# Optimization experiments

Hardware: AMD Instinct MI355X
Metric: run time of the kernel (lower is better)

Reference implementation:

```python
import jax, jax.numpy as jnp
import numpy as np

B, T, HH, WW, D, NH, MLPD, KH, KW = 2, 16, 24, 24, 128, 4, 512, 5, 5
T_ = T + 1
HW = HH * WW
SIZE = KH * KW
PH, PW = KH // 2, KW // 2


def _ln(x, w, b):
    m = x.mean(-1, keepdims=True)
    v = ((x - m) ** 2).mean(-1, keepdims=True)
    return (x - m) / jnp.sqrt(v + 1e-5) * w + b


def _mha(q, kv, mask, Wq, bq, Wk, bk, Wv, bv, Wo, bo):
    # q: (N, Lq, D), kv: (N, Lk, D), mask: (N, Lq|1, Lk) True = masked
    N, Lq, Dm = q.shape
    dh = Dm // NH
    qh = (q @ Wq + bq).reshape(N, Lq, NH, dh).transpose(0, 2, 1, 3)
    kh = (kv @ Wk + bk).reshape(N, -1, NH, dh).transpose(0, 2, 1, 3)
    vh = (kv @ Wv + bv).reshape(N, -1, NH, dh).transpose(0, 2, 1, 3)
    scores = jnp.einsum('nhqd,nhkd->nhqk', qh, kh) * (1.0 / np.sqrt(dh))
    logits = jnp.where(mask[:, None, :, :], -1e9, scores)
    attn = jax.nn.softmax(logits, axis=-1)
    out = jnp.einsum('nhqk,nhkd->nhqd', attn, vh).transpose(0, 2, 1, 3).reshape(N, Lq, Dm)
    return out @ Wo + bo, logits


def _unfold_patches(x):
    # x: (N, H, W, D) -> (N, H, W, SIZE, D), kernel positions row-major (matches F.unfold)
    xp = jnp.pad(x, ((0, 0), (PH, PH), (PW, PW), (0, 0)))
    return jnp.stack([xp[:, i:i + HH, j:j + WW, :] for i in range(KH) for j in range(KW)], axis=3)


def setup_inputs() -> dict:
    key = jax.random.key(0)
    ks = iter(jax.random.split(key, 48))
    w = lambda *s: jax.random.normal(next(ks), s, jnp.float32) * 0.02
    inp = {
        'query': jax.random.normal(next(ks), (B, T_, HW, D), jnp.float32),
        'spatial_mask': jnp.zeros((1,), bool),  # ignored by the module
        'temporal_mask': jnp.zeros((B * HW, T_, T_), bool),
        'ln_s_w': jnp.ones((D,), jnp.float32), 'ln_s_b': jnp.zeros((D,), jnp.float32),
        'sWq': w(D, D), 'sbq': jnp.zeros((D,), jnp.float32),
        'sWk': w(D, D), 'sbk': jnp.zeros((D,), jnp.float32),
        'sWv': w(D, D), 'sbv': jnp.zeros((D,), jnp.float32),
        'sWo': w(D, D), 'sbo': jnp.zeros((D,), jnp.float32),
        'ln_t_w': jnp.ones((D,), jnp.float32), 'ln_t_b': jnp.zeros((D,), jnp.float32),
        'tWq': w(D, D), 'tbq': jnp.zeros((D,), jnp.float32),
        'tWk': w(D, D), 'tbk': jnp.zeros((D,), jnp.float32),
        'tWv': w(D, D), 'tbv': jnp.zeros((D,), jnp.float32),
        'tWo': w(D, D), 'tbo': jnp.zeros((D,), jnp.float32),
        'ln_m_w': jnp.ones((D,), jnp.float32), 'ln_m_b': jnp.zeros((D,), jnp.float32),
        'mW1': w(D, MLPD), 'mb1': jnp.zeros((MLPD,), jnp.float32),
        'mW2': w(MLPD, D), 'mb2': jnp.zeros((D,), jnp.float32),
    }
    return inp


def reference(query, spatial_mask, temporal_mask, ln_s_w, ln_s_b, sWq, sbq, sWk, sbk, sWv, sbv, sWo, sbo,
              ln_t_w, ln_t_b, tWq, tbq, tWk, tbk, tWv, tbv, tWo, tbo, ln_m_w, ln_m_b, mW1, mb1, mW2, mb2):
    # ---- spatial branch (local window attention + global CLS key) ----
    visual = query[:, 1:].reshape(B * T, HH, WW, D)
    neigh = _unfold_patches(visual).reshape(B * T * HW, SIZE, D)
    vis = visual.reshape(B * T * HW, 1, D)
    cls = query[:, 0].mean(axis=1, keepdims=True)              # (B,1,D)
    cls_rep = jnp.tile(cls, (T * HW, 1, 1))                    # faithful to torch .repeat ordering
    kv = jnp.concatenate([cls_rep, neigh], axis=1)             # (N, SIZE+1, D)
    # padding mask: True where neighbor falls outside the frame (faithful: CLS zero-col appended LAST)
    valid = jnp.pad(jnp.ones((HH, WW), bool), ((PH, PH), (PW, PW)))
    mpat = jnp.stack([valid[i:i + HH, j:j + WW] for i in range(KH) for j in range(KW)], axis=2).reshape(HW, SIZE)
    smask = jnp.concatenate([~mpat, jnp.zeros((HW, 1), bool)], axis=1)           # (HW, SIZE+1)
    smask = jnp.broadcast_to(smask[None], (B * T, HW, SIZE + 1)).reshape(B * T * HW, 1, SIZE + 1)
    out, _ = _mha(_ln(vis, ln_s_w, ln_s_b), _ln(kv, ln_s_w, ln_s_b), smask,
                  sWq, sbq, sWk, sbk, sWv, sbv, sWo, sbo)
    x = out + vis
    x = jnp.concatenate([query[:, 0:1], x.reshape(B, T, HW, D)], axis=1)  # (B, T_, HW, D)
    # ---- temporal branch ----
    xt = x.transpose(0, 2, 1, 3).reshape(B * HW, T_, D)
    xn = _ln(xt, ln_t_w, ln_t_b)
    x_, logits = _mha(xn, xn, temporal_mask, tWq, tbq, tWk, tbk, tWv, tbv, tWo, tbo)
    xt = x_ + xt
    x = xt.reshape(B, HW, T_, D).transpose(0, 2, 1, 3)
    x = x.at[:, 0].set(x[:, 0:1].mean(axis=2))                 # average CLS across spatial locations
    logits = logits.reshape(B, HW, NH, T_, T_)
    # ---- MLP ----
    h = _ln(x, ln_m_w, ln_m_b)
    h = jax.nn.gelu(h @ mW1 + mb1, approximate=False) @ mW2 + mb2
    x = h + x
    return x, logits
```

## Files before the change

kernel.cpp:

```cpp
#include <hip/hip_runtime.h>
#include <math.h>

#define BB    2
#define TT    16
#define TP    17
#define HH_   24
#define WW_   24
#define HWW   576
#define DD    128
#define NHH   4
#define MLPD_ 512
#define NPIX  18432
#define NTOK  19584
#define SCALE 0.17677669529663688f
#define OUT0_SIZE 2506752

typedef unsigned short u16;
typedef __bf16 bf16x8 __attribute__((ext_vector_type(8)));
typedef float f32x4 __attribute__((ext_vector_type(4)));

__device__ __forceinline__ u16 f2b(float f) {
  unsigned u = __float_as_uint(f);
  u += 0x7FFFu + ((u >> 16) & 1u);
  return (u16)(u >> 16);
}
__device__ __forceinline__ float blo(unsigned u) { return __uint_as_float(u << 16); }
__device__ __forceinline__ float bhi(unsigned u) { return __uint_as_float(u & 0xFFFF0000u); }
__device__ __forceinline__ float b2f(u16 u) { return __uint_as_float((unsigned)u << 16); }

__device__ __forceinline__ float dot8p(uint4 a, uint4 b) {
  float s = blo(a.x) * blo(b.x) + bhi(a.x) * bhi(b.x);
  s += blo(a.y) * blo(b.y) + bhi(a.y) * bhi(b.y);
  s += blo(a.z) * blo(b.z) + bhi(a.z) * bhi(b.z);
  s += blo(a.w) * blo(b.w) + bhi(a.w) * bhi(b.w);
  return s;
}
__device__ __forceinline__ float getp(const float4* P, int j) {
  float4 v = P[j >> 2];
  switch (j & 3) { case 0: return v.x; case 1: return v.y; case 2: return v.z; default: return v.w; }
}
__device__ __forceinline__ void gld_lds16(const void* g, void* l) {
  __builtin_amdgcn_global_load_lds(
      (const __attribute__((address_space(1))) void*)g,
      (__attribute__((address_space(3))) void*)l, 16, 0, 0);
}

#define QLN8_BODY(SP, Q8, LNW, LNB, EMIT)                                        \
  {                                                                              \
    const float4* s4_ = (const float4*)(SP) + (Q8) * 4;                          \
    float4 xv_[4];                                                               \
    float sum_ = 0.f, sq_ = 0.f;                                                 \
    _Pragma("unroll")                                                            \
    for (int i_ = 0; i_ < 4; i_++) {                                             \
      float4 a_ = s4_[i_]; xv_[i_] = a_;                                         \
      sum_ += (a_.x + a_.y) + (a_.z + a_.w);                                     \
      sq_  += a_.x * a_.x + a_.y * a_.y + a_.z * a_.z + a_.w * a_.w;             \
    }                                                                            \
    sum_ += __shfl_xor(sum_, 1, 8); sum_ += __shfl_xor(sum_, 2, 8);              \
    sum_ += __shfl_xor(sum_, 4, 8);                                              \
    sq_  += __shfl_xor(sq_, 1, 8);  sq_  += __shfl_xor(sq_, 2, 8);               \
    sq_  += __shfl_xor(sq_, 4, 8);                                               \
    float mean_ = sum_ * (1.0f / DD);                                            \
    float inv_ = rsqrtf(sq_ * (1.0f / DD) - mean_ * mean_ + 1e-5f);              \
    const float4* w4_ = (const float4*)(LNW) + (Q8) * 4;                         \
    const float4* b4_ = (const float4*)(LNB) + (Q8) * 4;                         \
    _Pragma("unroll")                                                            \
    for (int i_ = 0; i_ < 2; i_++) {                                             \
      float4 a0_ = xv_[2 * i_], a1_ = xv_[2 * i_ + 1];                           \
      float4 w0_ = w4_[2 * i_], w1_ = w4_[2 * i_ + 1];                           \
      float4 c0_ = b4_[2 * i_], c1_ = b4_[2 * i_ + 1];                           \
      uint4 o_;                                                                  \
      o_.x = (unsigned)f2b((a0_.x - mean_) * inv_ * w0_.x + c0_.x)               \
           | ((unsigned)f2b((a0_.y - mean_) * inv_ * w0_.y + c0_.y) << 16);      \
      o_.y = (unsigned)f2b((a0_.z - mean_) * inv_ * w0_.z + c0_.z)               \
           | ((unsigned)f2b((a0_.w - mean_) * inv_ * w0_.w + c0_.w) << 16);      \
      o_.z = (unsigned)f2b((a1_.x - mean_) * inv_ * w1_.x + c1_.x)               \
           | ((unsigned)f2b((a1_.y - mean_) * inv_ * w1_.y + c1_.y) << 16);      \
      o_.w = (unsigned)f2b((a1_.z - mean_) * inv_ * w1_.z + c1_.z)               \
           | ((unsigned)f2b((a1_.w - mean_) * inv_ * w1_.w + c1_.w) << 16);      \
      EMIT(i_, o_);                                                              \
    }                                                                            \
  }

#define QLN_BODY(SP, Q, LNW, LNB, EMIT)                                          \
  {                                                                              \
    const float4* s4_ = (const float4*)(SP) + (Q) * 8;                           \
    float4 xv_[8];                                                               \
    float sum_ = 0.f, sq_ = 0.f;                                                 \
    _Pragma("unroll")                                                            \
    for (int i_ = 0; i_ < 8; i_++) {                                             \
      float4 a_ = s4_[i_]; xv_[i_] = a_;                                         \
      sum_ += (a_.x + a_.y) + (a_.z + a_.w);                                     \
      sq_  += a_.x * a_.x + a_.y * a_.y + a_.z * a_.z + a_.w * a_.w;             \
    }                                                                            \
    sum_ += __shfl_xor(sum_, 1, 4); sum_ += __shfl_xor(sum_, 2, 4);              \
    sq_  += __shfl_xor(sq_, 1, 4);  sq_  += __shfl_xor(sq_, 2, 4);               \
    float mean_ = sum_ * (1.0f / DD);                                            \
    float inv_ = rsqrtf(sq_ * (1.0f / DD) - mean_ * mean_ + 1e-5f);              \
    const float4* w4_ = (const float4*)(LNW) + (Q) * 8;                          \
    const float4* b4_ = (const float4*)(LNB) + (Q) * 8;                          \
    _Pragma("unroll")                                                            \
    for (int i_ = 0; i_ < 4; i_++) {                                             \
      float4 a0_ = xv_[2 * i_], a1_ = xv_[2 * i_ + 1];                           \
      float4 w0_ = w4_[2 * i_], w1_ = w4_[2 * i_ + 1];                           \
      float4 c0_ = b4_[2 * i_], c1_ = b4_[2 * i_ + 1];                           \
      uint4 o_;                                                                  \
      o_.x = (unsigned)f2b((a0_.x - mean_) * inv_ * w0_.x + c0_.x)               \
           | ((unsigned)f2b((a0_.y - mean_) * inv_ * w0_.y + c0_.y) << 16);      \
      o_.y = (unsigned)f2b((a0_.z - mean_) * inv_ * w0_.z + c0_.z)               \
           | ((unsigned)f2b((a0_.w - mean_) * inv_ * w0_.w + c0_.w) << 16);      \
      o_.z = (unsigned)f2b((a1_.x - mean_) * inv_ * w1_.x + c1_.x)               \
           | ((unsigned)f2b((a1_.y - mean_) * inv_ * w1_.y + c1_.y) << 16);      \
      o_.w = (unsigned)f2b((a1_.z - mean_) * inv_ * w1_.z + c1_.z)               \
           | ((unsigned)f2b((a1_.w - mean_) * inv_ * w1_.w + c1_.w) << 16);      \
      EMIT(i_, o_);                                                              \
    }                                                                            \
  }

#define MFMA_64x128(ASP, BSP, WR, WC, LANE, ACC)                                 \
  _Pragma("unroll")                                                              \
  for (int kc_ = 0; kc_ < 4; kc_++) {                                            \
    int kob_ = (kc_ * 32 + ((LANE) >> 4) * 8) * 2;                               \
    bf16x8 af_[2], bf_[2];                                                       \
    _Pragma("unroll")                                                            \
    for (int i_ = 0; i_ < 2; i_++) {                                             \
      int ra_ = (WR) * 32 + i_ * 16 + ((LANE) & 15);                             \
      af_[i_] = *(const bf16x8*)((const char*)(ASP) + ((ra_ * 256 + kob_) ^ ((ra_ & 7) << 4))); \
      int rb_ = (WC) * 32 + i_ * 16 + ((LANE) & 15);                             \
      bf_[i_] = *(const bf16x8*)((const char*)(BSP) + ((rb_ * 256 + kob_) ^ ((rb_ & 7) << 4))); \
    }                                                                            \
    _Pragma("unroll")                                                            \
    for (int i_ = 0; i_ < 2; i_++)                                               \
      _Pragma("unroll")                                                          \
      for (int j_ = 0; j_ < 2; j_++)                                             \
        ACC[i_][j_] = __builtin_amdgcn_mfma_f32_16x16x32_bf16(af_[i_], bf_[j_], ACC[i_][j_], 0, 0, 0); \
  }

__global__ void k_packprep(const float* w0, const float* w1, const float* w2, const float* w3,
                           const float* w4, const float* w5, const float* w6, const float* w7,
                           const float* w8, const float* w9,
                           const float* sbq, const float* sbk, const float* sbv,
                           const float* tbq, const float* tbk, const float* tbv,
                           const float* query, const float* ln_w, const float* ln_b,
                           u16* __restrict__ out, float* __restrict__ sb3, float* __restrict__ tb3,
                           u16* __restrict__ KCb, u16* __restrict__ VCb) {
  int bid = blockIdx.x, tid = threadIdx.x;
  if (bid < 1027) {
    int idx = bid * 256 + tid;
    if (idx < 131072) {
      int seg = idx >> 14, local = idx & 16383;
      const float* tbl[8] = {w0, w1, w2, w3, w4, w5, w6, w7};
      int kk = local >> 7, nn = local & 127;
      out[seg * 16384 + nn * 128 + kk] = f2b(tbl[seg][local]);
    } else if (idx < 196608) {
      int local = idx - 131072;
      int kk = local >> 9, nn = local & 511;
      out[131072 + nn * 128 + kk] = f2b(w8[local]);
    } else if (idx < 262144) {
      int local = idx - 196608;
      int kk = local >> 7, nn = local & 127;
      out[196608 + nn * 512 + kk] = f2b(w9[local]);
    } else if (idx < 262528) {
      int i = idx - 262144;
      sb3[i] = i < 128 ? sbq[i] : (i < 256 ? sbk[i - 128] : sbv[i - 256]);
    } else if (idx < 262912) {
      int i = idx - 262528;
      tb3[i] = i < 128 ? tbq[i] : (i < 256 ? tbk[i - 128] : tbv[i - 256]);
    }
    return;
  }
  __shared__ float part[2][DD];
  __shared__ float xr[DD];
  __shared__ float pk[2][DD], pv[2][DD];
  int r = bid - 1027;
  int c = tid >> 7, d = tid & 127;
  if (r < BB) {
    const float* base = query + (size_t)r * TP * HWW * DD + d;
    float s = 0.f;
    for (int hw = c * 288; hw < c * 288 + 288; ++hw) s += base[(size_t)hw * DD];
    part[c][d] = s;
    __syncthreads();
    if (tid < DD) part[0][tid] = (part[0][tid] + part[1][tid]) * (1.0f / HWW);
    __syncthreads();
    if (tid < DD) {
      float mean = 0.f;
      for (int i = 0; i < DD; i++) mean += part[0][i];
      mean *= (1.0f / DD);
      float var = 0.f;
      for (int i = 0; i < DD; i++) { float t = part[0][i] - mean; var += t * t; }
      var *= (1.0f / DD);
      xr[tid] = (part[0][tid] - mean) * rsqrtf(var + 1e-5f) * ln_w[tid] + ln_b[tid];
    }
  } else {
    if (tid < DD) xr[tid] = ln_b[tid];
  }
  __syncthreads();
  float sk = 0.f, sv = 0.f;
  for (int e = c * 64; e < c * 64 + 64; e++) {
    float xe = xr[e];
    sk += xe * w1[e * DD + d];
    sv += xe * w2[e * DD + d];
  }
  pk[c][d] = sk; pv[c][d] = sv;
  __syncthreads();
  if (tid < DD) {
    float k = pk[0][tid] + pk[1][tid] + sbk[tid];
    float v = pv[0][tid] + pv[1][tid] + sbv[tid];
    KCb[r * DD + tid] = f2b(k);
    VCb[r * DD + tid] = f2b(v);
  }
}

__global__ __launch_bounds__(256, 2) void k_gemm(
    const float* __restrict__ Av, const float* __restrict__ lnw, const float* __restrict__ lnb,
    const u16* __restrict__ Wt, const float* __restrict__ bias,
    u16* __restrict__ Cb, int ldc) {
  __shared__ __align__(16) u16 As[64 * 128];
  __shared__ __align__(16) u16 Bs[128 * 128];
  int tx = threadIdx.x;
  int row0 = blockIdx.x * 64, col0 = blockIdx.y * 128;
  int lane = tx & 63, wid = tx >> 6;
  f32x4 z = {0.f, 0.f, 0.f, 0.f};
  f32x4 acc[2][4];
#pragma unroll
  for (int i = 0; i < 2; i++)
#pragma unroll
    for (int j = 0; j < 4; j++) acc[i][j] = z;

  {
    int rloc = tx >> 2, q = tx & 3;
    int r = row0 + rloc;
    int b2 = r / (TT * HWW); int r2 = r - b2 * (TT * HWW);
    const float* sp = Av + ((size_t)b2 * TP * HWW + HWW + r2) * DD;
#define EMIT_AS(i_, o_) { int dstb = (rloc * 256 + q * 64 + (i_) * 16) ^ ((rloc & 7) << 4); \
                          *(uint4*)((char*)As + dstb) = o_; }
    QLN_BODY(sp, q, lnw, lnb, EMIT_AS)
#undef EMIT_AS
  }
#pragma unroll
  for (int t = 0; t < 8; t++) {
    int ci = t * 256 + tx;
    int r = ci >> 4;
    int c16 = (ci ^ (r & 7)) & 15;
    gld_lds16(&Wt[(size_t)(col0 + r) * 128 + c16 * 8], (char*)Bs + ci * 16);
  }
  __syncthreads();
#pragma unroll
  for (int kc = 0; kc < 4; kc++) {
    int kob = (kc * 32 + (lane >> 4) * 8) * 2;
    bf16x8 af[2], bfr[4];
#pragma unroll
    for (int i = 0; i < 2; i++) {
      int ra = (wid >> 1) * 32 + i * 16 + (lane & 15);
      af[i] = *(const bf16x8*)((const char*)As + ((ra * 256 + kob) ^ ((ra & 7) << 4)));
    }
#pragma unroll
    for (int j = 0; j < 4; j++) {
      int rb = (wid & 1) * 64 + j * 16 + (lane & 15);
      bfr[j] = *(const bf16x8*)((const char*)Bs + ((rb * 256 + kob) ^ ((rb & 7) << 4)));
    }
#pragma unroll
    for (int i = 0; i < 2; i++)
#pragma unroll
      for (int j = 0; j < 4; j++)
        acc[i][j] = __builtin_amdgcn_mfma_f32_16x16x32_bf16(af[i], bfr[j], acc[i][j], 0, 0, 0);
  }

  int rbase = row0 + (wid >> 1) * 32 + (lane >> 4) * 4;
  int cbase = col0 + (wid & 1) * 64 + (lane & 15);
#pragma unroll
  for (int i = 0; i < 2; i++)
#pragma unroll
    for (int e = 0; e < 4; e++) {
      int r = rbase + i * 16 + e;
#pragma unroll
      for (int j = 0; j < 4; j++) {
        int c = cbase + j * 16;
        Cb[(size_t)r * ldc + c] = f2b(acc[i][j][e] + bias[c]);
      }
    }
}

__global__ __launch_bounds__(512, 2) void k_f1(
    const u16* __restrict__ S0b, const float* __restrict__ query,
    const u16* __restrict__ WT, const float* __restrict__ sbo, const float* __restrict__ tb3,
    const float* __restrict__ lnw, const float* __restrict__ lnb,
    float* __restrict__ XB, u16* __restrict__ QKVb) {
  __shared__ __align__(16) char smem[50176];
  u16* As  = (u16*)smem;
  u16* Bs  = (u16*)(smem + 16384);
  float* L = (float*)smem;
  u16* As2 = (u16*)(smem + 33792);
  u16* Bs2 = (u16*)smem;
  int tx = threadIdx.x, bid = blockIdx.x;
  int lane = tx & 63, wid = tx >> 6;
  int wr = (wid >> 2) & 1, wc = wid & 3;
  f32x4 z = {0.f, 0.f, 0.f, 0.f};
  int rb0 = wr * 32 + (lane >> 4) * 4;
  int cb0 = wc * 32 + (lane & 15);
  size_t row0T;

  if (bid < 288) {
    int row0P = bid * 64;
    int b2 = row0P / (TT * HWW);
    row0T = (size_t)row0P + (size_t)(b2 + 1) * HWW;
#pragma unroll
    for (int t = 0; t < 2; t++) {
      int ci = t * 512 + tx; int r = ci >> 4; int c16 = (ci ^ (r & 7)) & 15;
      gld_lds16(&S0b[(size_t)(row0P + r) * 128 + c16 * 8], (char*)As + ci * 16);
    }
    const u16* Wo = WT + 49152;
#pragma unroll
    for (int t = 0; t < 4; t++) {
      int ci = t * 512 + tx; int r = ci >> 4; int c16 = (ci ^ (r & 7)) & 15;
      gld_lds16(&Wo[(size_t)r * 128 + c16 * 8], (char*)Bs + ci * 16);
    }
    __syncthreads();
    f32x4 acc[2][2];
#pragma unroll
    for (int i = 0; i < 2; i++)
#pragma unroll
      for (int j = 0; j < 2; j++) acc[i][j] = z;
    MFMA_64x128(As, Bs, wr, wc, lane, acc)
    __syncthreads();
#pragma unroll
    for (int i = 0; i < 2; i++)
#pragma unroll
      for (int e = 0; e < 4; e++) {
        int r = rb0 + i * 16 + e;
#pragma unroll
        for (int j = 0; j < 2; j++) {
          int c = cb0 + j * 16;
          float v = acc[i][j][e] + sbo[c] + query[(row0T + r) * DD + c];
          XB[(row0T + r) * DD + c] = v;
          L[r * 132 + c] = v;
        }
      }
    __syncthreads();
    int rloc = tx >> 3, q8 = tx & 7;
    const float* sp = L + rloc * 132;
#define EMIT_AS2(i_, o_) { int dstb = (rloc * 256 + q8 * 32 + (i_) * 16) ^ ((rloc & 7) << 4); \
                           *(uint4*)((char*)As2 + dstb) = o_; }
    QLN8_BODY(sp, q8, lnw, lnb, EMIT_AS2)
#undef EMIT_AS2
  } else {
    int pb = bid - 288;
    row0T = (size_t)(pb / 9) * TP * HWW + (size_t)(pb % 9) * 64;
    int rloc = tx >> 3, q8 = tx & 7;
    const float* sp = query + (row0T + rloc) * DD;
#define EMIT_AS2(i_, o_) { int dstb = (rloc * 256 + q8 * 32 + (i_) * 16) ^ ((rloc & 7) << 4); \
                           *(uint4*)((char*)As2 + dstb) = o_; }
    QLN8_BODY(sp, q8, lnw, lnb, EMIT_AS2)
#undef EMIT_AS2
  }
  __syncthreads();

  const u16* Wq = WT + 65536;
  for (int by = 0; by < 3; by++) {
    if (by) __syncthreads();
#pragma unroll
    for (int t = 0; t < 4; t++) {
      int ci = t * 512 + tx; int r = ci >> 4; int c16 = (ci ^ (r & 7)) & 15;
      gld_lds16(&Wq[(size_t)(by * 128 + r) * 128 + c16 * 8], (char*)Bs2 + ci * 16);
    }
    __syncthreads();
    f32x4 acc[2][2];
#pragma unroll
    for (int i = 0; i < 2; i++)
#pragma unroll
      for (int j = 0; j < 2; j++) acc[i][j] = z;
    MFMA_64x128(As2, Bs2, wr, wc, lane, acc)
#pragma unroll
    for (int i = 0; i < 2; i++)
#pragma unroll
      for (int e = 0; e < 4; e++) {
        int r = rb0 + i * 16 + e;
#pragma unroll
        for (int j = 0; j < 2; j++) {
          int c = cb0 + j * 16;
          QKVb[(row0T + r) * 384 + by * 128 + c] = f2b(acc[i][j][e] + tb3[by * 128 + c]);
        }
      }
  }
}

__global__ __launch_bounds__(512, 2) void k_f2(
    const u16* __restrict__ S0b, const float* __restrict__ XB, const float* __restrict__ query,
    const u16* __restrict__ WT, const float* __restrict__ tbo,
    const float* __restrict__ mb1, const float* __restrict__ mb2,
    const float* __restrict__ lnw, const float* __restrict__ lnb,
    float* __restrict__ X2, float* __restrict__ out0) {
  __shared__ __align__(16) char smem[66560];
  u16* As  = (u16*)smem;
  u16* Bs  = (u16*)(smem + 16384);
  float* L = (float*)smem;
  u16* As2 = (u16*)(smem + 33792);
  u16* Ws  = (u16*)smem;
  u16* Hs  = (u16*)(smem + 50176);
  int tx = threadIdx.x, bid = blockIdx.x;
  int lane = tx & 63, wid = tx >> 6;
  int wr = (wid >> 2) & 1, wc = wid & 3;
  bool isV = bid < 288;
  size_t row0T = isV ? ((size_t)(bid / 144) * TP * HWW + HWW + (size_t)(bid % 144) * 64)
                     : ((size_t)((bid - 288) / 9) * TP * HWW + (size_t)((bid - 288) % 9) * 64);
  f32x4 z = {0.f, 0.f, 0.f, 0.f};
  int rb0 = wr * 32 + (lane >> 4) * 4;
  int cb0 = wc * 32 + (lane & 15);

#pragma unroll
  for (int t = 0; t < 2; t++) {
    int ci = t * 512 + tx; int r = ci >> 4; int c16 = (ci ^ (r & 7)) & 15;
    gld_lds16(&S0b[(row0T + r) * 128 + c16 * 8], (char*)As + ci * 16);
  }
  const u16* Wo = WT + 114688;
#pragma unroll
  for (int t = 0; t < 4; t++) {
    int ci = t * 512 + tx; int r = ci >> 4; int c16 = (ci ^ (r & 7)) & 15;
    gld_lds16(&Wo[(size_t)r * 128 + c16 * 8], (char*)Bs + ci * 16);
  }
  __syncthreads();
  f32x4 acc[2][2];
#pragma unroll
  for (int i = 0; i < 2; i++)
#pragma unroll
    for (int j = 0; j < 2; j++) acc[i][j] = z;
  MFMA_64x128(As, Bs, wr, wc, lane, acc)
  __syncthreads();

  f32x4 xres[2][2];
  const float* res = isV ? XB : query;
#pragma unroll
  for (int i = 0; i < 2; i++)
#pragma unroll
    for (int e = 0; e < 4; e++) {
      int r = rb0 + i * 16 + e;
#pragma unroll
      for (int j = 0; j < 2; j++) {
        int c = cb0 + j * 16;
        float v = acc[i][j][e] + tbo[c] + res[(row0T + r) * DD + c];
        xres[i][j][e] = v;
        if (isV) L[r * 132 + c] = v;
        else     X2[(row0T + r) * DD + c] = v;
      }
    }
  if (!isV) return;
  __syncthreads();
  {
    int rloc = tx >> 3, q8 = tx & 7;
    const float* sp = L + rloc * 132;
#define EMIT_AS2(i_, o_) { int dstb = (rloc * 256 + q8 * 32 + (i_) * 16) ^ ((rloc & 7) << 4); \
                           *(uint4*)((char*)As2 + dstb) = o_; }
    QLN8_BODY(sp, q8, lnw, lnb, EMIT_AS2)
#undef EMIT_AS2
  }
  __syncthreads();

  const u16* W1 = WT + 131072;
  const u16* W2 = WT + 196608;
  f32x4 accC[2][2];
#pragma unroll
  for (int i = 0; i < 2; i++)
#pragma unroll
    for (int j = 0; j < 2; j++) accC[i][j] = z;

  for (int nb = 0; nb < 4; nb++) {
    if (nb) __syncthreads();
#pragma unroll
    for (int t = 0; t < 4; t++) {
      int ci = t * 512 + tx; int r = ci >> 4; int c16 = (ci ^ (r & 7)) & 15;
      gld_lds16(&W1[(size_t)(nb * 128 + r) * 128 + c16 * 8], (char*)Ws + ci * 16);
    }
    __syncthreads();
    f32x4 accH[2][2];
#pragma unroll
    for (int i = 0; i < 2; i++)
#pragma unroll
      for (int j = 0; j < 2; j++) accH[i][j] = z;
    MFMA_64x128(As2, Ws, wr, wc, lane, accH)
    __syncthreads();
#pragma unroll
    for (int i = 0; i < 2; i++)
#pragma unroll
      for (int e = 0; e < 4; e++) {
        int hr = rb0 + i * 16 + e;
#pragma unroll
        for (int j = 0; j < 2; j++) {
          int hc = cb0 + j * 16;
          float v = accH[i][j][e] + mb1[nb * 128 + hc];
          v = 0.5f * v * (1.0f + erff(v * 0.70710678118654752f));
          *(u16*)((char*)Hs + ((hr * 256 + hc * 2) ^ ((hr & 7) << 4))) = f2b(v);
        }
      }
#pragma unroll
    for (int t = 0; t < 4; t++) {
      int ci = t * 512 + tx; int r = ci >> 4; int c16 = (ci ^ (r & 7)) & 15;
      gld_lds16(&W2[(size_t)r * 512 + nb * 128 + c16 * 8], (char*)Ws + ci * 16);
    }
    __syncthreads();
    MFMA_64x128(Hs, Ws, wr, wc, lane, accC)
  }

#pragma unroll
  for (int i = 0; i < 2; i++)
#pragma unroll
    for (int e = 0; e < 4; e++) {
      int r = rb0 + i * 16 + e;
#pragma unroll
      for (int j = 0; j < 2; j++) {
        int c = cb0 + j * 16;
        out0[(row0T + r) * DD + c] = accC[i][j][e] + mb2[c] + xres[i][j][e];
      }
    }
}

__global__ __launch_bounds__(256) void k_sattn(const u16* __restrict__ qkvb,
                                               const u16* __restrict__ KCb,
                                               const u16* __restrict__ VCb,
                                               u16* __restrict__ outb) {
  __shared__ float Ps[8][32];
  int tid = threadIdx.x;
  int g = tid >> 5, lj = tid & 31;
  int bid = blockIdx.x;
  int blk = (bid & 7) * 1152 + (bid >> 3);
  int G = blk * 8 + g;
  int n = G >> 2, h = G & 3;
  int f = n / HWW, hw = n - f * HWW;
  int hp = hw / WW_, wp = hw - hp * WW_;
  size_t FB = (size_t)f * HWW * 384;

  const u16* kp;
  bool masked;
  if (lj == 0) {
    kp = KCb + (n & 1) * DD + h * 32;
    masked = !(hp >= 2 && wp >= 2);
  } else {
    int k = lj - 1;
    int y = hp + k / 5 - 2, x = wp + k % 5 - 2;
    bool vok = ((unsigned)y < 24u) & ((unsigned)x < 24u) & (k < 25);
    kp = vok ? (qkvb + FB + (size_t)(y * WW_ + x) * 384 + 128 + h * 32)
             : (KCb + BB * DD + h * 32);
    if (lj < 25) { int ym = hp + lj / 5 - 2, xm = wp + lj % 5 - 2;
                   masked = !(((unsigned)ym < 24u) & ((unsigned)xm < 24u)); }
    else masked = false;
  }
  const uint4* q4p = (const uint4*)(qkvb + (size_t)n * 384 + h * 32);
  const uint4* k4p = (const uint4*)kp;
  float s = 0.f;
#pragma unroll
  for (int i = 0; i < 4; i++) s += dot8p(q4p[i], k4p[i]);

  float scr = masked ? -1e9f : s * SCALE;
  if (lj >= 26) scr = -1e30f;
  float mx = scr;
#pragma unroll
  for (int o = 16; o > 0; o >>= 1) mx = fmaxf(mx, __shfl_xor(mx, o, 32));
  float p = __expf(scr - mx);
  float sum = p;
#pragma unroll
  for (int o = 16; o > 0; o >>= 1) sum += __shfl_xor(sum, o, 32);
  Ps[g][lj] = p * (1.0f / sum);

  float4 P4[7];
#pragma unroll
  for (int i = 0; i < 7; i++) P4[i] = *(const float4*)&Ps[g][i * 4];

  float o = getp(P4, 0) * b2f(VCb[(n & 1) * DD + h * 32 + lj]);
#pragma unroll
  for (int k = 0; k < 25; k++) {
    int y = hp + k / 5 - 2, x = wp + k % 5 - 2;
    bool vok = ((unsigned)y < 24u) & ((unsigned)x < 24u);
    const u16* vp = vok ? (qkvb + FB + (size_t)(y * WW_ + x) * 384 + 256)
                        : (VCb + BB * DD);
    o += getp(P4, k + 1) * b2f(vp[h * 32 + lj]);
  }
  outb[(size_t)n * DD + h * 32 + lj] = f2b(o);
}

__global__ __launch_bounds__(256) void k_tattn(const u16* __restrict__ qkv,
                                               u16* __restrict__ outb,
                                               float* __restrict__ logits) {
  __shared__ float Qs[8][TP][32];
  __shared__ float Ps[8][TP][17];
  int tid = threadIdx.x;
  int g = tid >> 5, lj = tid & 31;
  int s = blockIdx.x * 2 + (g >> 2);
  int h = g & 3;
  int b = s / HWW, hw = s - b * HWW;
  size_t base = ((size_t)b * TP * HWW + hw) * 384 + h * 32;
  const size_t TSTR = (size_t)HWW * 384;

  float kreg[32];
  {
    const uint4* k4 = (const uint4*)(qkv + base + (size_t)(lj < 17 ? lj : 16) * TSTR + 128);
#pragma unroll
    for (int i = 0; i < 4; i++) {
      uint4 u = k4[i];
      kreg[i * 8 + 0] = blo(u.x); kreg[i * 8 + 1] = bhi(u.x);
      kreg[i * 8 + 2] = blo(u.y); kreg[i * 8 + 3] = bhi(u.y);
      kreg[i * 8 + 4] = blo(u.z); kreg[i * 8 + 5] = bhi(u.z);
      kreg[i * 8 + 6] = blo(u.w); kreg[i * 8 + 7] = bhi(u.w);
    }
  }
  float vreg[TP];
#pragma unroll
  for (int t = 0; t < TP; t++) {
    Qs[g][t][lj] = b2f(qkv[base + (size_t)t * TSTR + lj]);
    vreg[t]      = b2f(qkv[base + (size_t)t * TSTR + 256 + lj]);
  }

  float* lp = logits + (size_t)s * (NHH * TP * TP) + (size_t)h * (TP * TP);
#pragma unroll 4
  for (int tq = 0; tq < TP; tq++) {
    const float4* qrow = (const float4*)&Qs[g][tq][0];
    float a0 = 0.f, a1 = 0.f, a2 = 0.f, a3 = 0.f;
#pragma unroll
    for (int d4 = 0; d4 < 8; d4++) {
      float4 q4 = qrow[d4];
      a0 += q4.x * kreg[d4 * 4 + 0];
      a1 += q4.y * kreg[d4 * 4 + 1];
      a2 += q4.z * kreg[d4 * 4 + 2];
      a3 += q4.w * kreg[d4 * 4 + 3];
    }
    float sc = ((a0 + a1) + (a2 + a3)) * SCALE;
    if (lj < 17) lp[tq * 17 + lj] = sc;
    float scm = (lj < 17) ? sc : -1e30f;
    float mx = scm;
#pragma unroll
    for (int o = 16; o > 0; o >>= 1) mx = fmaxf(mx, __shfl_xor(mx, o, 32));
    float p = __expf(scm - mx);
    float sum = p;
#pragma unroll
    for (int o = 16; o > 0; o >>= 1) sum += __shfl_xor(sum, o, 32);
    if (lj < 17) Ps[g][tq][lj] = p * (1.0f / sum);
  }
#pragma unroll 4
  for (int tq = 0; tq < TP; tq++) {
    const float* prow = &Ps[g][tq][0];
    float o = 0.f;
#pragma unroll
    for (int t = 0; t < TP; t++) o += prow[t] * vreg[t];
    size_t r = ((size_t)b * TP + tq) * HWW + hw;
    outb[r * DD + h * 32 + lj] = f2b(o);
  }
}

__global__ void k_f3(const float* __restrict__ x2,
                     const float* __restrict__ mW1, const float* __restrict__ mb1,
                     const float* __restrict__ mW2, const float* __restrict__ mb2,
                     const float* __restrict__ lnw, const float* __restrict__ lnb,
                     float* __restrict__ out0) {
  __shared__ float part[4][DD];
  __shared__ float cls[DD];
  __shared__ float lnr[DD];
  __shared__ float H[MLPD_];
  __shared__ float orow[DD];
  int b = blockIdx.x, tid = threadIdx.x;
  int c = tid >> 7, d = tid & 127;
  const float* base = x2 + (size_t)b * TP * HWW * DD;
  float s = 0.f;
  for (int hw = c * 144; hw < c * 144 + 144; ++hw) s += base[(size_t)hw * DD + d];
  part[c][d] = s;
  __syncthreads();
  if (tid < DD) cls[tid] = (part[0][tid] + part[1][tid] + part[2][tid] + part[3][tid]) * (1.0f / HWW);
  __syncthreads();
  if (tid < DD) {
    float mean = 0.f;
    for (int i = 0; i < DD; i++) mean += cls[i];
    mean *= (1.0f / DD);
    float var = 0.f;
    for (int i = 0; i < DD; i++) { float t = cls[i] - mean; var += t * t; }
    var *= (1.0f / DD);
    lnr[tid] = (cls[tid] - mean) * rsqrtf(var + 1e-5f) * lnw[tid] + lnb[tid];
  }
  __syncthreads();
  {
    float a = mb1[tid];
    for (int k = 0; k < DD; k++) a += lnr[k] * mW1[k * MLPD_ + tid];
    H[tid] = 0.5f * a * (1.0f + erff(a * 0.70710678118654752f));
  }
  __syncthreads();
  if (tid < DD) {
    float a = mb2[tid];
    for (int k = 0; k < MLPD_; k++) a += H[k] * mW2[k * DD + tid];
    orow[tid] = a + cls[tid];
  }
  __syncthreads();
  float* ob = out0 + (size_t)b * TP * HWW * DD;
  for (int idx = tid; idx < HWW * DD; idx += 512) ob[idx] = orow[idx & 127];
}

extern "C" void kernel_launch(void* const* d_in, const int* in_sizes, int n_in,
                              void* d_out, int out_size, void* d_ws, size_t ws_size,
                              hipStream_t stream) {
  const float* query  = (const float*)d_in[0];
  const float* ln_s_w = (const float*)d_in[3];
  const float* ln_s_b = (const float*)d_in[4];
  const float* sWq = (const float*)d_in[5];  const float* sbq = (const float*)d_in[6];
  const float* sWk = (const float*)d_in[7];  const float* sbk = (const float*)d_in[8];
  const float* sWv = (const float*)d_in[9];  const float* sbv = (const float*)d_in[10];
  const float* sWo = (const float*)d_in[11]; const float* sbo = (const float*)d_in[12];
  const float* ln_t_w = (const float*)d_in[13];
  const float* ln_t_b = (const float*)d_in[14];
  const float* tWq = (const float*)d_in[15]; const float* tbq = (const float*)d_in[16];
  const float* tWk = (const float*)d_in[17]; const float* tbk = (const float*)d_in[18];
  const float* tWv = (const float*)d_in[19]; const float* tbv = (const float*)d_in[20];
  const float* tWo = (const float*)d_in[21]; const float* tbo = (const float*)d_in[22];
  const float* ln_m_w = (const float*)d_in[23];
  const float* ln_m_b = (const float*)d_in[24];
  const float* mW1 = (const float*)d_in[25]; const float* mb1 = (const float*)d_in[26];
  const float* mW2 = (const float*)d_in[27]; const float* mb2 = (const float*)d_in[28];

  float* ws = (float*)d_ws;
  u16*   QKVb = (u16*)ws;
  u16*   S0b  = (u16*)(ws + 7520256);
  float* XB   = ws + 8773632;
  float* X2   = ws + 11280384;
  u16*   WT   = (u16*)(ws + 13787136);
  float* sb3  = ws + 13918208;
  float* tb3  = ws + 13918592;
  u16*   KCb  = (u16*)(ws + 13920000);
  u16*   VCb  = (u16*)(ws + 13920192);

  float* out0   = (float*)d_out;
  float* logits = out0 + OUT0_SIZE;

  k_packprep<<<1030, 256, 0, stream>>>(sWq, sWk, sWv, sWo, tWq, tWk, tWv, tWo, mW1, mW2,
                                       sbq, sbk, sbv, tbq, tbk, tbv,
                                       query, ln_s_w, ln_s_b, WT, sb3, tb3, KCb, VCb);
  k_gemm<<<dim3(288, 3), 256, 0, stream>>>(query, ln_s_w, ln_s_b, WT, sb3, QKVb, 384);
  k_sattn<<<9216, 256, 0, stream>>>(QKVb, KCb, VCb, S0b);
  k_f1<<<306, 512, 0, stream>>>(S0b, query, WT, sbo, tb3, ln_t_w, ln_t_b, XB, QKVb);
  k_tattn<<<BB * HWW / 2, 256, 0, stream>>>(QKVb, S0b, logits);
  k_f2<<<306, 512, 0, stream>>>(S0b, XB, query, WT, tbo, mb1, mb2, ln_m_w, ln_m_b, X2, out0);
  k_f3<<<2, 512, 0, stream>>>(X2, mW1, mb1, mW2, mb2, ln_m_w, ln_m_b, out0);
}
```

Measured before the change: 167.9 us.

## Halve row tile in fused f1/f2 kernels to 32 rows, use tanh GELU

```diff
diff --git a/kernel.cpp b/kernel.cpp
--- a/kernel.cpp
+++ b/kernel.cpp
@@ -43,6 +43,12 @@
   __builtin_amdgcn_global_load_lds(
       (const __attribute__((address_space(1))) void*)g,
       (__attribute__((address_space(3))) void*)l, 16, 0, 0);
+}
+__device__ __forceinline__ float fgelu(float x) {
+  float u = x * (0.7978845608028654f + 0.03567740814f * x * x);
+  u = fminf(fmaxf(u, -15.f), 15.f);
+  float e = __expf(2.0f * u);
+  return x * e / (e + 1.0f);
 }
 
 #define QLN8_BODY(SP, Q8, LNW, LNB, EMIT)                                        \
@@ -117,23 +123,18 @@
     }                                                                            \
   }
 
-#define MFMA_64x128(ASP, BSP, WR, WC, LANE, ACC)                                 \
+#define MFMA_32x128(ASP, BSP, WR, WC, LANE, ACC)                                 \
   _Pragma("unroll")                                                              \
   for (int kc_ = 0; kc_ < 4; kc_++) {                                            \
     int kob_ = (kc_ * 32 + ((LANE) >> 4) * 8) * 2;                               \
-    bf16x8 af_[2], bf_[2];                                                       \
+    int ra_ = (WR) * 16 + ((LANE) & 15);                                         \
+    bf16x8 af_ = *(const bf16x8*)((const char*)(ASP) + ((ra_ * 256 + kob_) ^ ((ra_ & 7) << 4))); \
     _Pragma("unroll")                                                            \
-    for (int i_ = 0; i_ < 2; i_++) {                                             \
-      int ra_ = (WR) * 32 + i_ * 16 + ((LANE) & 15);                             \
-      af_[i_] = *(const bf16x8*)((const char*)(ASP) + ((ra_ * 256 + kob_) ^ ((ra_ & 7) << 4))); \
-      int rb_ = (WC) * 32 + i_ * 16 + ((LANE) & 15);                             \
-      bf_[i_] = *(const bf16x8*)((const char*)(BSP) + ((rb_ * 256 + kob_) ^ ((rb_ & 7) << 4))); \
+    for (int j_ = 0; j_ < 4; j_++) {                                             \
+      int rb_ = (WC) * 64 + j_ * 16 + ((LANE) & 15);                             \
+      bf16x8 bf_ = *(const bf16x8*)((const char*)(BSP) + ((rb_ * 256 + kob_) ^ ((rb_ & 7) << 4))); \
+      ACC[j_] = __builtin_amdgcn_mfma_f32_16x16x32_bf16(af_, bf_, ACC[j_], 0, 0, 0); \
     }                                                                            \
-    _Pragma("unroll")                                                            \
-    for (int i_ = 0; i_ < 2; i_++)                                               \
-      _Pragma("unroll")                                                          \
-      for (int j_ = 0; j_ < 2; j_++)                                             \
-        ACC[i_][j_] = __builtin_amdgcn_mfma_f32_16x16x32_bf16(af_[i_], bf_[j_], ACC[i_][j_], 0, 0, 0); \
   }
 
 __global__ void k_packprep(const float* w0, const float* w1, const float* w2, const float* w3,
@@ -281,61 +282,56 @@
     }
 }
 
-__global__ __launch_bounds__(512, 2) void k_f1(
+__global__ __launch_bounds__(256, 3) void k_f1(
     const u16* __restrict__ S0b, const float* __restrict__ query,
     const u16* __restrict__ WT, const float* __restrict__ sbo, const float* __restrict__ tb3,
     const float* __restrict__ lnw, const float* __restrict__ lnb,
     float* __restrict__ XB, u16* __restrict__ QKVb) {
-  __shared__ __align__(16) char smem[50176];
+  __shared__ __align__(16) char smem[49152];
   u16* As  = (u16*)smem;
-  u16* Bs  = (u16*)(smem + 16384);
+  u16* Bs  = (u16*)(smem + 8192);
   float* L = (float*)smem;
-  u16* As2 = (u16*)(smem + 33792);
-  u16* Bs2 = (u16*)smem;
+  u16* As2 = (u16*)(smem + 40960);
   int tx = threadIdx.x, bid = blockIdx.x;
   int lane = tx & 63, wid = tx >> 6;
-  int wr = (wid >> 2) & 1, wc = wid & 3;
+  int wr = wid >> 1, wc = wid & 1;
   f32x4 z = {0.f, 0.f, 0.f, 0.f};
-  int rb0 = wr * 32 + (lane >> 4) * 4;
-  int cb0 = wc * 32 + (lane & 15);
+  int rb0 = wr * 16 + (lane >> 4) * 4;
+  int cb0 = wc * 64 + (lane & 15);
   size_t row0T;
 
-  if (bid < 288) {
-    int row0P = bid * 64;
+  if (bid < 576) {
+    int row0P = bid * 32;
     int b2 = row0P / (TT * HWW);
     row0T = (size_t)row0P + (size_t)(b2 + 1) * HWW;
 #pragma unroll
     for (int t = 0; t < 2; t++) {
-      int ci = t * 512 + tx; int r = ci >> 4; int c16 = (ci ^ (r & 7)) & 15;
+      int ci = t * 256 + tx; int r = ci >> 4; int c16 = (ci ^ (r & 7)) & 15;
       gld_lds16(&S0b[(size_t)(row0P + r) * 128 + c16 * 8], (char*)As + ci * 16);
     }
     const u16* Wo = WT + 49152;
 #pragma unroll
-    for (int t = 0; t < 4; t++) {
-      int ci = t * 512 + tx; int r = ci >> 4; int c16 = (ci ^ (r & 7)) & 15;
+    for (int t = 0; t < 8; t++) {
+      int ci = t * 256 + tx; int r = ci >> 4; int c16 = (ci ^ (r & 7)) & 15;
       gld_lds16(&Wo[(size_t)r * 128 + c16 * 8], (char*)Bs + ci * 16);
     }
     __syncthreads();
-    f32x4 acc[2][2];
-#pragma unroll
-    for (int i = 0; i < 2; i++)
-#pragma unroll
-      for (int j = 0; j < 2; j++) acc[i][j] = z;
-    MFMA_64x128(As, Bs, wr, wc, lane, acc)
-    __syncthreads();
-#pragma unroll
-    for (int i = 0; i < 2; i++)
-#pragma unroll
-      for (int e = 0; e < 4; e++) {
-        int r = rb0 + i * 16 + e;
-#pragma unroll
-        for (int j = 0; j < 2; j++) {
-          int c = cb0 + j * 16;
-          float v = acc[i][j][e] + sbo[c] + query[(row0T + r) * DD + c];
-          XB[(row0T + r) * DD + c] = v;
-          L[r * 132 + c] = v;
-        }
+    f32x4 acc[4];
+#pragma unroll
+    for (int j = 0; j < 4; j++) acc[j] = z;
+    MFMA_32x128(As, Bs, wr, wc, lane, acc)
+    __syncthreads();
+#pragma unroll
+    for (int e = 0; e < 4; e++) {
+      int r = rb0 + e;
+#pragma unroll
+      for (int j = 0; j < 4; j++) {
+        int c = cb0 + j * 16;
+        float v = acc[j][e] + sbo[c] + query[(row0T + r) * DD + c];
+        XB[(row0T + r) * DD + c] = v;
+        L[r * 132 + c] = v;
       }
+    }
     __syncthreads();
     int rloc = tx >> 3, q8 = tx & 7;
     const float* sp = L + rloc * 132;
@@ -344,8 +340,8 @@
     QLN8_BODY(sp, q8, lnw, lnb, EMIT_AS2)
 #undef EMIT_AS2
   } else {
-    int pb = bid - 288;
-    row0T = (size_t)(pb / 9) * TP * HWW + (size_t)(pb % 9) * 64;
+    int pb = bid - 576;
+    row0T = (size_t)(pb / 18) * TP * HWW + (size_t)(pb % 18) * 32;
     int rloc = tx >> 3, q8 = tx & 7;
     const float* sp = query + (row0T + rloc) * DD;
 #define EMIT_AS2(i_, o_) { int dstb = (rloc * 256 + q8 * 32 + (i_) * 16) ^ ((rloc & 7) << 4); \
@@ -359,90 +355,81 @@
   for (int by = 0; by < 3; by++) {
     if (by) __syncthreads();
 #pragma unroll
-    for (int t = 0; t < 4; t++) {
-      int ci = t * 512 + tx; int r = ci >> 4; int c16 = (ci ^ (r & 7)) & 15;
-      gld_lds16(&Wq[(size_t)(by * 128 + r) * 128 + c16 * 8], (char*)Bs2 + ci * 16);
-    }
-    __syncthreads();
-    f32x4 acc[2][2];
-#pragma unroll
-    for (int i = 0; i < 2; i++)
-#pragma unroll
-      for (int j = 0; j < 2; j++) acc[i][j] = z;
-    MFMA_64x128(As2, Bs2, wr, wc, lane, acc)
-#pragma unroll
-    for (int i = 0; i < 2; i++)
-#pragma unroll
-      for (int e = 0; e < 4; e++) {
-        int r = rb0 + i * 16 + e;
-#pragma unroll
-        for (int j = 0; j < 2; j++) {
-          int c = cb0 + j * 16;
-          QKVb[(row0T + r) * 384 + by * 128 + c] = f2b(acc[i][j][e] + tb3[by * 128 + c]);
-        }
+    for (int t = 0; t < 8; t++) {
+      int ci = t * 256 + tx; int r = ci >> 4; int c16 = (ci ^ (r & 7)) & 15;
+      gld_lds16(&Wq[(size_t)(by * 128 + r) * 128 + c16 * 8], (char*)Bs + ci * 16);
+    }
+    __syncthreads();
+    f32x4 acc[4];
+#pragma unroll
+    for (int j = 0; j < 4; j++) acc[j] = z;
+    MFMA_32x128(As2, Bs, wr, wc, lane, acc)
+#pragma unroll
+    for (int e = 0; e < 4; e++) {
+      int r = rb0 + e;
+#pragma unroll
+      for (int j = 0; j < 4; j++) {
+        int c = cb0 + j * 16;
+        QKVb[(row0T + r) * 384 + by * 128 + c] = f2b(acc[j][e] + tb3[by * 128 + c]);
       }
-  }
-}
-
-__global__ __launch_bounds__(512, 2) void k_f2(
+    }
+  }
+}
+
+__global__ __launch_bounds__(256, 3) void k_f2(
     const u16* __restrict__ S0b, const float* __restrict__ XB, const float* __restrict__ query,
     const u16* __restrict__ WT, const float* __restrict__ tbo,
     const float* __restrict__ mb1, const float* __restrict__ mb2,
     const float* __restrict__ lnw, const float* __restrict__ lnb,
     float* __restrict__ X2, float* __restrict__ out0) {
-  __shared__ __align__(16) char smem[66560];
+  __shared__ __align__(16) char smem[49152];
   u16* As  = (u16*)smem;
-  u16* Bs  = (u16*)(smem + 16384);
+  u16* Bs  = (u16*)(smem + 8192);
   float* L = (float*)smem;
-  u16* As2 = (u16*)(smem + 33792);
-  u16* Ws  = (u16*)smem;
-  u16* Hs  = (u16*)(smem + 50176);
+  u16* As2 = (u16*)(smem + 40960);
+  u16* Hs  = (u16*)smem;
   int tx = threadIdx.x, bid = blockIdx.x;
   int lane = tx & 63, wid = tx >> 6;
-  int wr = (wid >> 2) & 1, wc = wid & 3;
-  bool isV = bid < 288;
-  size_t row0T = isV ? ((size_t)(bid / 144) * TP * HWW + HWW + (size_t)(bid % 144) * 64)
-                     : ((size_t)((bid - 288) / 9) * TP * HWW + (size_t)((bid - 288) % 9) * 64);
+  int wr = wid >> 1, wc = wid & 1;
+  bool isV = bid < 576;
+  size_t row0T = isV ? ((size_t)(bid / 288) * TP * HWW + HWW + (size_t)(bid % 288) * 32)
+                     : ((size_t)((bid - 576) / 18) * TP * HWW + (size_t)((bid - 576) % 18) * 32);
   f32x4 z = {0.f, 0.f, 0.f, 0.f};
-  int rb0 = wr * 32 + (lane >> 4) * 4;
-  int cb0 = wc * 32 + (lane & 15);
+  int rb0 = wr * 16 + (lane >> 4) * 4;
+  int cb0 = wc * 64 + (lane & 15);
 
 #pragma unroll
   for (int t = 0; t < 2; t++) {
-    int ci = t * 512 + tx; int r = ci >> 4; int c16 = (ci ^ (r & 7)) & 15;
+    int ci = t * 256 + tx; int r = ci >> 4; int c16 = (ci ^ (r & 7)) & 15;
     gld_lds16(&S0b[(row0T + r) * 128 + c16 * 8], (char*)As + ci * 16);
   }
   const u16* Wo = WT + 114688;
 #pragma unroll
-  for (int t = 0; t < 4; t++) {
-    int ci = t * 512 + tx; int r = ci >> 4; int c16 = (ci ^ (r & 7)) & 15;
+  for (int t = 0; t < 8; t++) {
+    int ci = t * 256 + tx; int r = ci >> 4; int c16 = (ci ^ (r & 7)) & 15;
     gld_lds16(&Wo[(size_t)r * 128 + c16 * 8], (char*)Bs + ci * 16);
   }
   __syncthreads();
-  f32x4 acc[2][2];
-#pragma unroll
-  for (int i = 0; i < 2; i++)
-#pragma unroll
-    for (int j = 0; j < 2; j++) acc[i][j] = z;
-  MFMA_64x128(As, Bs, wr, wc, lane, acc)
-  __syncthreads();
-
-  f32x4 xres[2][2];
+  f32x4 acc[4];
+#pragma unroll
+  for (int j = 0; j < 4; j++) acc[j] = z;
+  MFMA_32x128(As, Bs, wr, wc, lane, acc)
+  __syncthreads();
+
+  f32x4 xres[4];
   const float* res = isV ? XB : query;
 #pragma unroll
-  for (int i = 0; i < 2; i++)
-#pragma unroll
-    for (int e = 0; e < 4; e++) {
-      int r = rb0 + i * 16 + e;
-#pragma unroll
-      for (int j = 0; j < 2; j++) {
-        int c = cb0 + j * 16;
-        float v = acc[i][j][e] + tbo[c] + res[(row0T + r) * DD + c];
-        xres[i][j][e] = v;
-        if (isV) L[r * 132 + c] = v;
-        else     X2[(row0T + r) * DD + c] = v;
-      }
-    }
+  for (int e = 0; e < 4; e++) {
+    int r = rb0 + e;
+#pragma unroll
+    for (int j = 0; j < 4; j++) {
+      int c = cb0 + j * 16;
+      float v = acc[j][e] + tbo[c] + res[(row0T + r) * DD + c];
+      xres[j][e] = v;
+      if (isV) L[r * 132 + c] = v;
+      else     X2[(row0T + r) * DD + c] = v;
+    }
+  }
   if (!isV) return;
   __syncthreads();
   {
@@ -457,60 +444,51 @@
 
   const u16* W1 = WT + 131072;
   const u16* W2 = WT + 196608;
-  f32x4 accC[2][2];
-#pragma unroll
-  for (int i = 0; i < 2; i++)
-#pragma unroll
-    for (int j = 0; j < 2; j++) accC[i][j] = z;
+  f32x4 accC[4];
+#pragma unroll
+  for (int j = 0; j < 4; j++) accC[j] = z;
 
   for (int nb = 0; nb < 4; nb++) {
     if (nb) __syncthreads();
 #pragma unroll
-    for (int t = 0; t < 4; t++) {
-      int ci = t * 512 + tx; int r = ci >> 4; int c16 = (ci ^ (r & 7)) & 15;
-      gld_lds16(&W1[(size_t)(nb * 128 + r) * 128 + c16 * 8], (char*)Ws + ci * 16);
-    }
-    __syncthreads();
-    f32x4 accH[2][2];
-#pragma unroll
-    for (int i = 0; i < 2; i++)
-#pragma unroll
-      for (int j = 0; j < 2; j++) accH[i][j] = z;
-    MFMA_64x128(As2, Ws, wr, wc, lane, accH)
-    __syncthreads();
-#pragma unroll
-    for (int i = 0; i < 2; i++)
-#pragma unroll
-      for (int e = 0; e < 4; e++) {
-        int hr = rb0 + i * 16 + e;
-#pragma unroll
-        for (int j = 0; j < 2; j++) {
-          int hc = cb0 + j * 16;
-          float v = accH[i][j][e] + mb1[nb * 128 + hc];
-          v = 0.5f * v * (1.0f + erff(v * 0.70710678118654752f));
-          *(u16*)((char*)Hs + ((hr * 256 + hc * 2) ^ ((hr & 7) << 4))) = f2b(v);
-        }
+    for (int t = 0; t < 8; t++) {
+      int ci = t * 256 + tx; int r = ci >> 4; int c16 = (ci ^ (r & 7)) & 15;
+      gld_lds16(&W1[(size_t)(nb * 128 + r) * 128 + c16 * 8], (char*)Bs + ci * 16);
+    }
+    __syncthreads();
+    f32x4 accH[4];
+#pragma unroll
+    for (int j = 0; j < 4; j++) accH[j] = z;
+    MFMA_32x128(As2, Bs, wr, wc, lane, accH)
+    __syncthreads();
+#pragma unroll
+    for (int e = 0; e < 4; e++) {
+      int hr = rb0 + e;
+#pragma unroll
+      for (int j = 0; j < 4; j++) {
+        int hc = cb0 + j * 16;
+        float v = fgelu(accH[j][e] + mb1[nb * 128 + hc]);
+        *(u16*)((char*)Hs + ((hr * 256 + hc * 2) ^ ((hr & 7) << 4))) = f2b(v);
       }
-#pragma unroll
-    for (int t = 0; t < 4; t++) {
-      int ci = t * 512 + tx; int r = ci >> 4; int c16 = (ci ^ (r & 7)) & 15;
-      gld_lds16(&W2[(size_t)r * 512 + nb * 128 + c16 * 8], (char*)Ws + ci * 16);
-    }
-    __syncthreads();
-    MFMA_64x128(Hs, Ws, wr, wc, lane, accC)
-  }
-
-#pragma unroll
-  for (int i = 0; i < 2; i++)
-#pragma unroll
-    for (int e = 0; e < 4; e++) {
-      int r = rb0 + i * 16 + e;
-#pragma unroll
-      for (int j = 0; j < 2; j++) {
-        int c = cb0 + j * 16;
-        out0[(row0T + r) * DD + c] = accC[i][j][e] + mb2[c] + xres[i][j][e];
-      }
-    }
+    }
+#pragma unroll
+    for (int t = 0; t < 8; t++) {
+      int ci = t * 256 + tx; int r = ci >> 4; int c16 = (ci ^ (r & 7)) & 15;
+      gld_lds16(&W2[(size_t)r * 512 + nb * 128 + c16 * 8], (char*)Bs + ci * 16);
+    }
+    __syncthreads();
+    MFMA_32x128(Hs, Bs, wr, wc, lane, accC)
+  }
+
+#pragma unroll
+  for (int e = 0; e < 4; e++) {
+    int r = rb0 + e;
+#pragma unroll
+    for (int j = 0; j < 4; j++) {
+      int c = cb0 + j * 16;
+      out0[(row0T + r) * DD + c] = accC[j][e] + mb2[c] + xres[j][e];
+    }
+  }
 }
 
 __global__ __launch_bounds__(256) void k_sattn(const u16* __restrict__ qkvb,
@@ -729,8 +707,8 @@
                                        query, ln_s_w, ln_s_b, WT, sb3, tb3, KCb, VCb);
   k_gemm<<<dim3(288, 3), 256, 0, stream>>>(query, ln_s_w, ln_s_b, WT, sb3, QKVb, 384);
   k_sattn<<<9216, 256, 0, stream>>>(QKVb, KCb, VCb, S0b);
-  k_f1<<<306, 512, 0, stream>>>(S0b, query, WT, sbo, tb3, ln_t_w, ln_t_b, XB, QKVb);
+  k_f1<<<612, 256, 0, stream>>>(S0b, query, WT, sbo, tb3, ln_t_w, ln_t_b, XB, QKVb);
   k_tattn<<<BB * HWW / 2, 256, 0, stream>>>(QKVb, S0b, logits);
-  k_f2<<<306, 512, 0, stream>>>(S0b, XB, query, WT, tbo, mb1, mb2, ln_m_w, ln_m_b, X2, out0);
+  k_f2<<<612, 256, 0, stream>>>(S0b, XB, query, WT, tbo, mb1, mb2, ln_m_w, ln_m_b, X2, out0);
   k_f3<<<2, 512, 0, stream>>>(X2, mW1, mb1, mW2, mb2, ln_m_w, ln_m_b, out0);
 }
```

Measured after the change: 156.8 us (median of 2 runs). 1.07x faster.
